# Kernel optimization log

Measured on AMD Instinct MI355X. Metric: run time of the kernel, lower is better.

Reference implementation:

```python
import jax, jax.numpy as jnp
import numpy as np

K = 2                 # top-k experts per token
CAP_FACTOR = 1.25     # capacity factor


def setup_inputs() -> dict:
    key = jax.random.key(0)
    ks = jax.random.split(key, 6)
    B, T, C, H, E = 8, 2048, 1024, 4096, 8
    return {
        "x":  jax.random.normal(ks[0], (B, T, C), dtype=jnp.float32),
        "Wr": jax.random.normal(ks[1], (C, E), dtype=jnp.float32) * 0.02,
        "W1": jax.random.normal(ks[2], (E, C, H), dtype=jnp.float32) * 0.02,
        "b1": jax.random.normal(ks[3], (E, H), dtype=jnp.float32) * 0.02,
        "W2": jax.random.normal(ks[4], (E, H, C), dtype=jnp.float32) * 0.02,
        "b2": jax.random.normal(ks[5], (E, C), dtype=jnp.float32) * 0.02,
    }


def reference(x, Wr, W1, b1, W2, b2):
    B, T, C = x.shape
    E = Wr.shape[1]
    capacity = int(T / E * CAP_FACTOR)  # per (expert, batch-row) bucket, as in torch code

    # Router: probs over experts, top-k selection
    probs = jax.nn.softmax(x @ Wr, axis=-1)                  # [B,T,E]
    topk_probs, topk_experts = jax.lax.top_k(probs, K)       # [B,T,K]

    # Flatten token slots in (t, k) order -- matches torch nonzero() enumeration
    S = T * K
    e_flat = topk_experts.reshape(B, S)                      # [B,S] int32
    p_flat = topk_probs.reshape(B, S)                        # [B,S]
    x_rep = jnp.repeat(x, K, axis=1)                         # [B,S,C]; slot (t,k) -> x[b,t]

    # Position of each slot within its (batch-row b, expert e) group
    onehot = jax.nn.one_hot(e_flat, E, dtype=jnp.int32)      # [B,S,E]
    pos_all = jnp.cumsum(onehot, axis=1) - onehot            # position before self
    pos = jnp.take_along_axis(pos_all, e_flat[..., None], axis=-1)[..., 0]  # [B,S]
    keep = pos < capacity                                    # tokens beyond capacity dropped
    pos_c = jnp.minimum(pos, capacity - 1)

    # Dispatch: scatter kept tokens into [E, B, capacity, C] buffer (padding_val = 0)
    b_idx = jnp.broadcast_to(jnp.arange(B)[:, None], (B, S))
    buf = jnp.zeros((E, B, capacity, C), dtype=x.dtype)
    buf = buf.at[e_flat, b_idx, pos_c].add(x_rep * keep[..., None].astype(x.dtype))

    # Expert FFN (grouped GEMM): Linear -> ReLU -> Linear, one weight set per expert
    h = jax.nn.relu(jnp.einsum('ebnc,ech->ebnh', buf, W1) + b1[:, None, None, :])
    y = jnp.einsum('ebnh,ehc->ebnc', h, W2) + b2[:, None, None, :]

    # Combine: gather back, zero dropped slots, weight by router prob, sum over k
    y_tok = y[e_flat, b_idx, pos_c]                          # [B,S,C]
    y_tok = y_tok * (keep[..., None].astype(x.dtype)) * p_flat[..., None]
    out = y_tok.reshape(B, T, K, C).sum(axis=2)              # [B,T,C]
    return out
```

## Files before the change

### kernel.cpp

```cpp
#include <hip/hip_runtime.h>

#define B_ 8
#define T_ 2048
#define C_ 1024
#define H_ 4096
#define E_ 8
#define S_ (2 * T_)
#define CAP 320
#define ME 2560
#define NROWS (E_ * ME)

typedef __attribute__((ext_vector_type(8))) short short8;
typedef __attribute__((ext_vector_type(4))) float f32x4;

__device__ __forceinline__ unsigned short f2bf(float f) {
  unsigned u = __float_as_uint(f);
  unsigned r = 0x7FFFu + ((u >> 16) & 1u);
  return (unsigned short)((u + r) >> 16);
}
__device__ __forceinline__ float bf2f(unsigned short u) {
  return __uint_as_float(((unsigned)u) << 16);
}

__device__ __forceinline__ void gload_lds16(const void* g, void* l) {
  __builtin_amdgcn_global_load_lds(
      (const __attribute__((address_space(1))) unsigned int*)g,
      (__attribute__((address_space(3))) unsigned int*)l, 16, 0, 0);
}

__global__ void cvt_transpose(const float* __restrict__ in,
                              unsigned short* __restrict__ out, int R, int Cc) {
  __shared__ float t[64][65];
  const int tid = threadIdx.x;
  const long eoff = (long)blockIdx.z * R * Cc;
  const int r0 = blockIdx.x * 64, c0 = blockIdx.y * 64;
#pragma unroll
  for (int it = 0; it < 4; ++it) {
    int r = it * 16 + (tid >> 4);
    int c = (tid & 15) * 4;
    float4 v = *(const float4*)(in + eoff + (long)(r0 + r) * Cc + c0 + c);
    t[r][c] = v.x; t[r][c + 1] = v.y; t[r][c + 2] = v.z; t[r][c + 3] = v.w;
  }
  __syncthreads();
#pragma unroll
  for (int it = 0; it < 4; ++it) {
    int oc = it * 16 + (tid >> 4);
    int orr = (tid & 15) * 4;
    union { unsigned short u[4]; unsigned long long ll; } o;
    o.u[0] = f2bf(t[orr + 0][oc]); o.u[1] = f2bf(t[orr + 1][oc]);
    o.u[2] = f2bf(t[orr + 2][oc]); o.u[3] = f2bf(t[orr + 3][oc]);
    *(unsigned long long*)(out + eoff + (long)(c0 + oc) * R + r0 + orr) = o.ll;
  }
}

__global__ void router_cvt(const float* __restrict__ x, const float* __restrict__ Wr,
                           int* __restrict__ es, float* __restrict__ ps,
                           unsigned short* __restrict__ x_bf) {
  const int token = blockIdx.x * 4 + (threadIdx.x >> 6);
  const int lane = threadIdx.x & 63;
  const float* xr = x + (long)token * C_;
  float acc[8] = {0, 0, 0, 0, 0, 0, 0, 0};
#pragma unroll
  for (int j = 0; j < 4; ++j) {
    int c = j * 256 + lane * 4;
    float4 xv = *(const float4*)(xr + c);
    union { unsigned short u[4]; unsigned long long ll; } o;
    o.u[0] = f2bf(xv.x); o.u[1] = f2bf(xv.y); o.u[2] = f2bf(xv.z); o.u[3] = f2bf(xv.w);
    *(unsigned long long*)(x_bf + (long)token * C_ + c) = o.ll;
    const float xe[4] = {xv.x, xv.y, xv.z, xv.w};
#pragma unroll
    for (int i = 0; i < 4; ++i) {
      const float4* wr = (const float4*)(Wr + (long)(c + i) * 8);
      float4 w0 = wr[0], w1 = wr[1];
      float v = xe[i];
      acc[0] += v * w0.x; acc[1] += v * w0.y; acc[2] += v * w0.z; acc[3] += v * w0.w;
      acc[4] += v * w1.x; acc[5] += v * w1.y; acc[6] += v * w1.z; acc[7] += v * w1.w;
    }
  }
#pragma unroll
  for (int off = 32; off >= 1; off >>= 1)
#pragma unroll
    for (int e = 0; e < 8; ++e) acc[e] += __shfl_xor(acc[e], off);
  float mx = acc[0];
#pragma unroll
  for (int e = 1; e < 8; ++e) mx = fmaxf(mx, acc[e]);
  float pr[8], se = 0.f;
#pragma unroll
  for (int e = 0; e < 8; ++e) { pr[e] = expf(acc[e] - mx); se += pr[e]; }
  float inv = 1.f / se;
  int e0 = 0; float v0 = pr[0];
#pragma unroll
  for (int e = 1; e < 8; ++e) if (pr[e] > v0) { v0 = pr[e]; e0 = e; }
  int e1 = -1; float v1 = -1.f;
#pragma unroll
  for (int e = 0; e < 8; ++e) if (e != e0 && pr[e] > v1) { v1 = pr[e]; e1 = e; }
  if (lane == 0) {
    es[2 * token] = e0;     ps[2 * token] = v0 * inv;
    es[2 * token + 1] = e1; ps[2 * token + 1] = v1 * inv;
  }
}

__global__ void positions(const int* __restrict__ es, int* __restrict__ pos,
                          int* __restrict__ tsrc) {
  const int b = blockIdx.x;
  const int lane = threadIdx.x;
  int cnt[8] = {0, 0, 0, 0, 0, 0, 0, 0};
  unsigned long long below = (1ULL << lane) - 1ULL;
  int e_next = es[(long)b * S_ + lane];
  for (int chunk = 0; chunk < S_ / 64; ++chunk) {
    int e = e_next;
    if (chunk + 1 < S_ / 64) e_next = es[(long)b * S_ + (chunk + 1) * 64 + lane];
    int myPos = 0;
#pragma unroll
    for (int ei = 0; ei < 8; ++ei) {
      unsigned long long m = __ballot(e == ei);
      if (e == ei) myPos = cnt[ei] + __popcll(m & below);
      cnt[ei] += __popcll(m);
    }
    int s = chunk * 64 + lane;
    pos[(long)b * S_ + s] = myPos;
    if (myPos < CAP)
      tsrc[(long)e * ME + b * CAP + myPos] = b * T_ + (s >> 1);
  }
}

template <bool GATHER, bool RELU>
__global__ __launch_bounds__(256, 3) void moe_gemm(
    const unsigned short* __restrict__ A, const unsigned short* __restrict__ BT,
    const float* __restrict__ bias, const int* __restrict__ tsrc,
    unsigned short* __restrict__ outp, const int Kdim, const int N, const int NT) {
  constexpr int BM = 128, BN = 128, BK = 64;
  constexpr int MT = ME / BM;
  __shared__ unsigned short As[BM * BK];
  __shared__ unsigned short Bs[BN * BK];
  const int tid = threadIdx.x, lane = tid & 63, w = tid >> 6;

  const int nwg = E_ * NT * MT;
  const int chunk = nwg >> 3;
  const int swz = (blockIdx.x & 7) * chunk + (blockIdx.x >> 3);
  const int e = swz / (NT * MT);
  const int rem = swz % (NT * MT);
  const int nt = rem / MT, mt = rem % MT;
  const int n0 = nt * BN;

  const unsigned short* aPtr[4];
#pragma unroll
  for (int i = 0; i < 4; ++i) {
    int ra = w * 32 + i * 8 + (lane >> 3);
    int j = lane & 7;
    long rowbase;
    if constexpr (GATHER) {
      int xrow = tsrc[(long)e * ME + mt * BM + ra];
      if (xrow < 0) xrow = 0;
      rowbase = (long)xrow * Kdim;
    } else {
      rowbase = ((long)e * ME + mt * BM + ra) * (long)Kdim;
    }
    aPtr[i] = A + rowbase + ((j ^ (ra & 7)) << 3);
  }
  const unsigned short* bPtr[4];
#pragma unroll
  for (int i = 0; i < 4; ++i) {
    int rb = w * 32 + i * 8 + (lane >> 3);
    int j = lane & 7;
    bPtr[i] = BT + ((long)e * N + n0 + rb) * (long)Kdim + ((j ^ (rb & 7)) << 3);
  }

  const int wm = w >> 1, wn = w & 1;
  f32x4 acc[4][4];
#pragma unroll
  for (int m = 0; m < 4; ++m)
#pragma unroll
    for (int n = 0; n < 4; ++n) acc[m][n] = (f32x4){0.f, 0.f, 0.f, 0.f};

  int arow[4], brow[4];
#pragma unroll
  for (int i = 0; i < 4; ++i) {
    arow[i] = wm * 64 + i * 16 + (lane & 15);
    brow[i] = wn * 64 + i * 16 + (lane & 15);
  }
  const int jjb = lane >> 4;

  for (int kt = 0; kt < Kdim / BK; ++kt) {
#pragma unroll
    for (int i = 0; i < 4; ++i)
      gload_lds16(aPtr[i], &As[(w * 32 + i * 8) * BK]);
#pragma unroll
    for (int i = 0; i < 4; ++i)
      gload_lds16(bPtr[i], &Bs[(w * 32 + i * 8) * BK]);
#pragma unroll
    for (int i = 0; i < 4; ++i) { aPtr[i] += BK; bPtr[i] += BK; }
    __syncthreads();
#pragma unroll
    for (int s = 0; s < 2; ++s) {
      short8 af[4], bf[4];
#pragma unroll
      for (int m = 0; m < 4; ++m) {
        int slot = (s * 4 + jjb) ^ (arow[m] & 7);
        af[m] = *(const short8*)&As[arow[m] * BK + slot * 8];
      }
#pragma unroll
      for (int n = 0; n < 4; ++n) {
        int slot = (s * 4 + jjb) ^ (brow[n] & 7);
        bf[n] = *(const short8*)&Bs[brow[n] * BK + slot * 8];
      }
#pragma unroll
      for (int m = 0; m < 4; ++m)
#pragma unroll
        for (int n = 0; n < 4; ++n)
          acc[m][n] = __builtin_amdgcn_mfma_f32_16x16x32_bf16(af[m], bf[n],
                                                              acc[m][n], 0, 0, 0);
    }
    __syncthreads();
  }

  const long rbase = (long)e * ME + mt * BM;
#pragma unroll
  for (int m = 0; m < 4; ++m) {
#pragma unroll
    for (int n = 0; n < 4; ++n) {
      const int trow = wm * 64 + m * 16 + ((lane >> 4) << 2);
      const int col = n0 + wn * 64 + n * 16 + (lane & 15);
      const float bv = bias[(long)e * N + col];
#pragma unroll
      for (int j = 0; j < 4; ++j) {
        float v = acc[m][n][j] + bv;
        if constexpr (RELU) v = fmaxf(v, 0.f);
        outp[(rbase + trow + j) * N + col] = f2bf(v);
      }
    }
  }
}

__global__ void combine(const unsigned short* __restrict__ y,
                        const int* __restrict__ es, const float* __restrict__ ps,
                        const int* __restrict__ pos, float* __restrict__ out) {
  const int token = blockIdx.x;
  const int b = token >> 11;
  const int s0 = 2 * token, s1 = s0 + 1;
  int e0 = es[s0], e1 = es[s1];
  int q0 = pos[s0], q1 = pos[s1];
  float p0 = ps[s0], p1 = ps[s1];
  const bool k0 = q0 < CAP, k1 = q1 < CAP;
  if (q0 > CAP - 1) q0 = CAP - 1;
  if (q1 > CAP - 1) q1 = CAP - 1;
  const unsigned short* r0 = y + ((long)e0 * ME + b * CAP + q0) * C_;
  const unsigned short* r1 = y + ((long)e1 * ME + b * CAP + q1) * C_;
  const int c = threadIdx.x * 4;
  float4 a = {0.f, 0.f, 0.f, 0.f};
  if (k0) {
    union { unsigned short u[4]; unsigned long long ll; } v;
    v.ll = *(const unsigned long long*)(r0 + c);
    a.x += p0 * bf2f(v.u[0]); a.y += p0 * bf2f(v.u[1]);
    a.z += p0 * bf2f(v.u[2]); a.w += p0 * bf2f(v.u[3]);
  }
  if (k1) {
    union { unsigned short u[4]; unsigned long long ll; } v;
    v.ll = *(const unsigned long long*)(r1 + c);
    a.x += p1 * bf2f(v.u[0]); a.y += p1 * bf2f(v.u[1]);
    a.z += p1 * bf2f(v.u[2]); a.w += p1 * bf2f(v.u[3]);
  }
  *(float4*)(out + (long)token * C_ + c) = a;
}

extern "C" void kernel_launch(void* const* d_in, const int* in_sizes, int n_in,
                              void* d_out, int out_size, void* d_ws, size_t ws_size,
                              hipStream_t stream) {
  const float* x = (const float*)d_in[0];
  const float* Wr = (const float*)d_in[1];
  const float* W1 = (const float*)d_in[2];
  const float* b1 = (const float*)d_in[3];
  const float* W2 = (const float*)d_in[4];
  const float* b2 = (const float*)d_in[5];
  float* out = (float*)d_out;
  char* ws = (char*)d_ws;
  unsigned short* x_bf = (unsigned short*)(ws + 0L);
  unsigned short* W1T = (unsigned short*)(ws + 33554432L);
  unsigned short* W2T = (unsigned short*)(ws + 100663296L);
  unsigned short* h = (unsigned short*)(ws + 167772160L);
  unsigned short* y = (unsigned short*)(ws + 335544320L);
  int* es = (int*)(ws + 377487360L);
  float* ps = (float*)(ws + 377618432L);
  int* pos = (int*)(ws + 377749504L);
  int* tsrc = (int*)(ws + 377880576L);

  cvt_transpose<<<dim3(16, 64, 8), 256, 0, stream>>>(W1, W1T, C_, H_);
  cvt_transpose<<<dim3(64, 16, 8), 256, 0, stream>>>(W2, W2T, H_, C_);
  router_cvt<<<4096, 256, 0, stream>>>(x, Wr, es, ps, x_bf);
  hipMemsetAsync(tsrc, 0xFF, NROWS * sizeof(int), stream);
  positions<<<8, 64, 0, stream>>>(es, pos, tsrc);
  moe_gemm<true, true><<<5120, 256, 0, stream>>>(x_bf, W1T, b1, tsrc, h, C_, H_, 32);
  moe_gemm<false, false><<<1280, 256, 0, stream>>>(h, W2T, b2, nullptr, y, H_, C_, 8);
  combine<<<16384, 256, 0, stream>>>(y, es, ps, pos, out);
}
```

Before: 565.1 us.

## Use 256x256 double-buffered GEMM tiles with split-K for second expert GEMM

Replaces the 128x128 single-buffered expert GEMM with a 512-thread 256x256 tile kernel. It double-buffers LDS, issuing the next K-tile's loads between MFMA groups, and raises wave priority around the MFMA blocks. The second GEMM is split along K into two halves so it fills more workgroups, and the combine kernel sums the two partial outputs. This trades more LDS and registers per block, and an extra bf16 partial-output read in combine, for higher data reuse and better latency hiding.

```diff
diff --git a/kernel.cpp b/kernel.cpp
--- a/kernel.cpp
+++ b/kernel.cpp
@@ -125,108 +125,146 @@
 }
 
 template <bool GATHER, bool RELU>
-__global__ __launch_bounds__(256, 3) void moe_gemm(
+__global__ __launch_bounds__(512, 2) void moe_gemm256(
     const unsigned short* __restrict__ A, const unsigned short* __restrict__ BT,
     const float* __restrict__ bias, const int* __restrict__ tsrc,
-    unsigned short* __restrict__ outp, const int Kdim, const int N, const int NT) {
-  constexpr int BM = 128, BN = 128, BK = 64;
-  constexpr int MT = ME / BM;
-  __shared__ unsigned short As[BM * BK];
-  __shared__ unsigned short Bs[BN * BK];
+    unsigned short* __restrict__ outp, const int Kfull, const int Kslice,
+    const int NT, const int KS) {
+  constexpr int BK = 64;
+  constexpr int MT = ME / 256;
+  __shared__ unsigned short As[2][256 * BK];
+  __shared__ unsigned short Bs[2][256 * BK];
   const int tid = threadIdx.x, lane = tid & 63, w = tid >> 6;
-
-  const int nwg = E_ * NT * MT;
+  const int wr = w >> 2, wc = w & 3;
+  const int N = NT * 256;
+
+  const int nwg = E_ * KS * NT * MT;
   const int chunk = nwg >> 3;
   const int swz = (blockIdx.x & 7) * chunk + (blockIdx.x >> 3);
-  const int e = swz / (NT * MT);
-  const int rem = swz % (NT * MT);
-  const int nt = rem / MT, mt = rem % MT;
-  const int n0 = nt * BN;
+  const int mt = swz % MT;
+  int rem = swz / MT;
+  const int nt = rem % NT; rem /= NT;
+  const int ks = rem % KS;
+  const int e = rem / KS;
+  const int n0 = nt * 256;
+  const long ksoff = (long)ks * Kslice;
 
   const unsigned short* aPtr[4];
 #pragma unroll
-  for (int i = 0; i < 4; ++i) {
-    int ra = w * 32 + i * 8 + (lane >> 3);
-    int j = lane & 7;
-    long rowbase;
-    if constexpr (GATHER) {
-      int xrow = tsrc[(long)e * ME + mt * BM + ra];
-      if (xrow < 0) xrow = 0;
-      rowbase = (long)xrow * Kdim;
-    } else {
-      rowbase = ((long)e * ME + mt * BM + ra) * (long)Kdim;
-    }
-    aPtr[i] = A + rowbase + ((j ^ (ra & 7)) << 3);
-  }
+  for (int hh = 0; hh < 2; ++hh)
+#pragma unroll
+    for (int i = 0; i < 2; ++i) {
+      int r = hh * 128 + i * 64 + w * 8 + (lane >> 3);
+      int p = lane & 7;
+      long rowbase;
+      if constexpr (GATHER) {
+        int xrow = tsrc[(long)e * ME + mt * 256 + r];
+        if (xrow < 0) xrow = 0;
+        rowbase = (long)xrow * Kfull;
+      } else {
+        rowbase = ((long)e * ME + mt * 256 + r) * (long)Kfull;
+      }
+      aPtr[hh * 2 + i] = A + rowbase + ksoff + ((p ^ (r & 7)) << 3);
+    }
   const unsigned short* bPtr[4];
 #pragma unroll
-  for (int i = 0; i < 4; ++i) {
-    int rb = w * 32 + i * 8 + (lane >> 3);
-    int j = lane & 7;
-    bPtr[i] = BT + ((long)e * N + n0 + rb) * (long)Kdim + ((j ^ (rb & 7)) << 3);
-  }
-
-  const int wm = w >> 1, wn = w & 1;
-  f32x4 acc[4][4];
-#pragma unroll
-  for (int m = 0; m < 4; ++m)
+  for (int hh = 0; hh < 2; ++hh)
+#pragma unroll
+    for (int i = 0; i < 2; ++i) {
+      int r = hh * 128 + i * 64 + w * 8 + (lane >> 3);
+      int p = lane & 7;
+      bPtr[hh * 2 + i] =
+          BT + ((long)e * N + n0 + r) * (long)Kfull + ksoff + ((p ^ (r & 7)) << 3);
+    }
+
+  f32x4 acc[8][4];
+#pragma unroll
+  for (int m = 0; m < 8; ++m)
 #pragma unroll
     for (int n = 0; n < 4; ++n) acc[m][n] = (f32x4){0.f, 0.f, 0.f, 0.f};
 
-  int arow[4], brow[4];
-#pragma unroll
-  for (int i = 0; i < 4; ++i) {
-    arow[i] = wm * 64 + i * 16 + (lane & 15);
-    brow[i] = wn * 64 + i * 16 + (lane & 15);
-  }
-  const int jjb = lane >> 4;
-
-  for (int kt = 0; kt < Kdim / BK; ++kt) {
-#pragma unroll
-    for (int i = 0; i < 4; ++i)
-      gload_lds16(aPtr[i], &As[(w * 32 + i * 8) * BK]);
-#pragma unroll
-    for (int i = 0; i < 4; ++i)
-      gload_lds16(bPtr[i], &Bs[(w * 32 + i * 8) * BK]);
-#pragma unroll
-    for (int i = 0; i < 4; ++i) { aPtr[i] += BK; bPtr[i] += BK; }
+  const int l15 = lane & 15, l4 = lane >> 4;
+
+#pragma unroll
+  for (int hh = 0; hh < 2; ++hh)
+#pragma unroll
+    for (int i = 0; i < 2; ++i) {
+      gload_lds16(aPtr[hh * 2 + i], &As[0][(hh * 128 + i * 64 + w * 8) * BK]);
+      gload_lds16(bPtr[hh * 2 + i], &Bs[0][(hh * 128 + i * 64 + w * 8) * BK]);
+    }
+  __syncthreads();
+
+  const int nkt = Kslice / BK;
+  int cur = 0;
+  for (int kt = 0; kt < nkt; ++kt) {
+    const bool pf = (kt + 1 < nkt);
+    const long koff = (long)(kt + 1) * BK;
+    short8 bfr[4][2];
+#pragma unroll
+    for (int q = 0; q < 4; ++q) {
+      if (q == 0) {
+#pragma unroll
+        for (int n = 0; n < 4; ++n)
+#pragma unroll
+          for (int s = 0; s < 2; ++s) {
+            int r = wc * 64 + n * 16 + l15;
+            int slot = (s * 4 + l4) ^ (r & 7);
+            bfr[n][s] = *(const short8*)&Bs[cur][r * BK + slot * 8];
+          }
+      }
+      short8 af[2][2];
+#pragma unroll
+      for (int mi = 0; mi < 2; ++mi)
+#pragma unroll
+        for (int s = 0; s < 2; ++s) {
+          int r = wr * 128 + (q * 2 + mi) * 16 + l15;
+          int slot = (s * 4 + l4) ^ (r & 7);
+          af[mi][s] = *(const short8*)&As[cur][r * BK + slot * 8];
+        }
+      if (pf) {
+        if (q < 2) {
+          gload_lds16(aPtr[q * 2 + 0] + koff,
+                      &As[cur ^ 1][(q * 128 + 0 + w * 8) * BK]);
+          gload_lds16(aPtr[q * 2 + 1] + koff,
+                      &As[cur ^ 1][(q * 128 + 64 + w * 8) * BK]);
+        } else {
+          gload_lds16(bPtr[(q - 2) * 2 + 0] + koff,
+                      &Bs[cur ^ 1][((q - 2) * 128 + 0 + w * 8) * BK]);
+          gload_lds16(bPtr[(q - 2) * 2 + 1] + koff,
+                      &Bs[cur ^ 1][((q - 2) * 128 + 64 + w * 8) * BK]);
+        }
+      }
+      asm volatile("s_waitcnt lgkmcnt(0)" ::: "memory");
+      __builtin_amdgcn_sched_barrier(0);
+      __builtin_amdgcn_s_setprio(1);
+#pragma unroll
+      for (int mi = 0; mi < 2; ++mi)
+#pragma unroll
+        for (int n = 0; n < 4; ++n)
+#pragma unroll
+          for (int s = 0; s < 2; ++s)
+            acc[q * 2 + mi][n] = __builtin_amdgcn_mfma_f32_16x16x32_bf16(
+                af[mi][s], bfr[n][s], acc[q * 2 + mi][n], 0, 0, 0);
+      __builtin_amdgcn_s_setprio(0);
+      __builtin_amdgcn_sched_barrier(0);
+    }
     __syncthreads();
-#pragma unroll
-    for (int s = 0; s < 2; ++s) {
-      short8 af[4], bf[4];
-#pragma unroll
-      for (int m = 0; m < 4; ++m) {
-        int slot = (s * 4 + jjb) ^ (arow[m] & 7);
-        af[m] = *(const short8*)&As[arow[m] * BK + slot * 8];
-      }
-#pragma unroll
-      for (int n = 0; n < 4; ++n) {
-        int slot = (s * 4 + jjb) ^ (brow[n] & 7);
-        bf[n] = *(const short8*)&Bs[brow[n] * BK + slot * 8];
-      }
-#pragma unroll
-      for (int m = 0; m < 4; ++m)
-#pragma unroll
-        for (int n = 0; n < 4; ++n)
-          acc[m][n] = __builtin_amdgcn_mfma_f32_16x16x32_bf16(af[m], bf[n],
-                                                              acc[m][n], 0, 0, 0);
-    }
-    __syncthreads();
-  }
-
-  const long rbase = (long)e * ME + mt * BM;
-#pragma unroll
-  for (int m = 0; m < 4; ++m) {
+    cur ^= 1;
+  }
+
+  const long rbase = (long)ks * NROWS + (long)e * ME + mt * 256;
+#pragma unroll
+  for (int m = 0; m < 8; ++m) {
 #pragma unroll
     for (int n = 0; n < 4; ++n) {
-      const int trow = wm * 64 + m * 16 + ((lane >> 4) << 2);
-      const int col = n0 + wn * 64 + n * 16 + (lane & 15);
-      const float bv = bias[(long)e * N + col];
+      const int trow = wr * 128 + m * 16 + (l4 << 2);
+      const int col = n0 + wc * 64 + n * 16 + l15;
+      const float bv = (ks == 0) ? bias[(long)e * N + col] : 0.f;
 #pragma unroll
       for (int j = 0; j < 4; ++j) {
         float v = acc[m][n][j] + bv;
         if constexpr (RELU) v = fmaxf(v, 0.f);
-        outp[(rbase + trow + j) * N + col] = f2bf(v);
+        outp[(rbase + trow + j) * (long)N + col] = f2bf(v);
       }
     }
   }
@@ -244,21 +282,28 @@
   const bool k0 = q0 < CAP, k1 = q1 < CAP;
   if (q0 > CAP - 1) q0 = CAP - 1;
   if (q1 > CAP - 1) q1 = CAP - 1;
+  const long half = (long)NROWS * C_;
   const unsigned short* r0 = y + ((long)e0 * ME + b * CAP + q0) * C_;
   const unsigned short* r1 = y + ((long)e1 * ME + b * CAP + q1) * C_;
   const int c = threadIdx.x * 4;
   float4 a = {0.f, 0.f, 0.f, 0.f};
   if (k0) {
-    union { unsigned short u[4]; unsigned long long ll; } v;
+    union { unsigned short u[4]; unsigned long long ll; } v, vv;
     v.ll = *(const unsigned long long*)(r0 + c);
-    a.x += p0 * bf2f(v.u[0]); a.y += p0 * bf2f(v.u[1]);
-    a.z += p0 * bf2f(v.u[2]); a.w += p0 * bf2f(v.u[3]);
+    vv.ll = *(const unsigned long long*)(r0 + half + c);
+    a.x += p0 * (bf2f(v.u[0]) + bf2f(vv.u[0]));
+    a.y += p0 * (bf2f(v.u[1]) + bf2f(vv.u[1]));
+    a.z += p0 * (bf2f(v.u[2]) + bf2f(vv.u[2]));
+    a.w += p0 * (bf2f(v.u[3]) + bf2f(vv.u[3]));
   }
   if (k1) {
-    union { unsigned short u[4]; unsigned long long ll; } v;
+    union { unsigned short u[4]; unsigned long long ll; } v, vv;
     v.ll = *(const unsigned long long*)(r1 + c);
-    a.x += p1 * bf2f(v.u[0]); a.y += p1 * bf2f(v.u[1]);
-    a.z += p1 * bf2f(v.u[2]); a.w += p1 * bf2f(v.u[3]);
+    vv.ll = *(const unsigned long long*)(r1 + half + c);
+    a.x += p1 * (bf2f(v.u[0]) + bf2f(vv.u[0]));
+    a.y += p1 * (bf2f(v.u[1]) + bf2f(vv.u[1]));
+    a.z += p1 * (bf2f(v.u[2]) + bf2f(vv.u[2]));
+    a.w += p1 * (bf2f(v.u[3]) + bf2f(vv.u[3]));
   }
   *(float4*)(out + (long)token * C_ + c) = a;
 }
@@ -279,17 +324,19 @@
   unsigned short* W2T = (unsigned short*)(ws + 100663296L);
   unsigned short* h = (unsigned short*)(ws + 167772160L);
   unsigned short* y = (unsigned short*)(ws + 335544320L);
-  int* es = (int*)(ws + 377487360L);
-  float* ps = (float*)(ws + 377618432L);
-  int* pos = (int*)(ws + 377749504L);
-  int* tsrc = (int*)(ws + 377880576L);
+  int* es = (int*)(ws + 419430400L);
+  float* ps = (float*)(ws + 419561472L);
+  int* pos = (int*)(ws + 419692544L);
+  int* tsrc = (int*)(ws + 419823616L);
 
   cvt_transpose<<<dim3(16, 64, 8), 256, 0, stream>>>(W1, W1T, C_, H_);
   cvt_transpose<<<dim3(64, 16, 8), 256, 0, stream>>>(W2, W2T, H_, C_);
   router_cvt<<<4096, 256, 0, stream>>>(x, Wr, es, ps, x_bf);
   hipMemsetAsync(tsrc, 0xFF, NROWS * sizeof(int), stream);
   positions<<<8, 64, 0, stream>>>(es, pos, tsrc);
-  moe_gemm<true, true><<<5120, 256, 0, stream>>>(x_bf, W1T, b1, tsrc, h, C_, H_, 32);
-  moe_gemm<false, false><<<1280, 256, 0, stream>>>(h, W2T, b2, nullptr, y, H_, C_, 8);
+  moe_gemm256<true, true><<<1280, 512, 0, stream>>>(x_bf, W1T, b1, tsrc, h,
+                                                    C_, C_, 16, 1);
+  moe_gemm256<false, false><<<640, 512, 0, stream>>>(h, W2T, b2, nullptr, y,
+                                                     H_, H_ / 2, 4, 2);
   combine<<<16384, 256, 0, stream>>>(y, es, ps, pos, out);
 }
```

Result: slower. 578.2 us (+2.3%).
